# Kernel tuning notes

Hardware: AMD Instinct MI355X
Metric: run time of the kernel (lower is better)

The kernel has to match this reference:

```python
import jax, jax.numpy as jnp
import numpy as np

OUT_F = 4096
IN_F = 4096
NUM_BITS = 4
BLOCK = 64
R = 16
LORA_SCALE = 32.0 / R  # lora_alpha / r


def setup_inputs() -> dict:
    key = jax.random.key(0)
    k1, k2, k3, k4, k5, k6 = jax.random.split(key, 6)
    n_packed = OUT_F * IN_F * NUM_BITS // 8  # bytes; 2 nibbles per byte
    n_blocks = OUT_F * IN_F // BLOCK
    return {
        "x": jax.random.normal(k1, (2, 1024, IN_F), dtype=jnp.float32),
        "qweight": jax.random.randint(k2, (n_packed,), 0, 256, dtype=jnp.int32),
        "scales": jax.random.uniform(k3, (n_blocks,), dtype=jnp.float32),
        "bias": jax.random.normal(k4, (OUT_F,), dtype=jnp.float32),
        "lora_A": jax.random.normal(k5, (R, IN_F), dtype=jnp.float32) * 0.02,
        "lora_B": jax.random.normal(k6, (OUT_F, R), dtype=jnp.float32) * 0.02,
    }


def _dequantize(qweight, scales):
    # uniform 4-bit lookup table: linspace(-1, 1, 16)
    table = jnp.linspace(-1.0, 1.0, 2 ** NUM_BITS).astype(scales.dtype)
    mask = (1 << NUM_BITS) - 1
    # unpack: index i stored at bits [i*NUM_BITS, (i+1)*NUM_BITS) of each byte
    lo = qweight & mask
    hi = (qweight >> NUM_BITS) & mask
    idx = jnp.stack([lo, hi], axis=-1).reshape(-1)  # [OUT_F*IN_F]
    vals = table[idx]                                # gather from lookup table
    # per-block rescale, then reshape to [OUT_F, IN_F]
    w = vals.reshape(-1, BLOCK) * scales[:, None]
    return w.reshape(OUT_F, IN_F)


def reference(x, qweight, scales, bias, lora_A, lora_B):
    W = _dequantize(qweight, scales)                      # [out, in]
    base = jnp.einsum('bsi,oi->bso', x, W) + bias          # F.linear
    lora = jnp.einsum('bsr,or->bso', jnp.einsum('bsi,ri->bsr', x, lora_A), lora_B)
    return base + LORA_SCALE * lora
```

## Files before the change

kernel.cpp:

```cpp
#include <hip/hip_runtime.h>
#include <hip/hip_bf16.h>
#include <stdint.h>

#define IN_F   4096
#define OUT_F  4096
#define M_ROWS 2048
#define LORA_SCALE 2.0f

typedef __bf16 bf16x8 __attribute__((ext_vector_type(8)));
typedef float  f32x4  __attribute__((ext_vector_type(4)));

typedef const __attribute__((address_space(1))) void gvoid_t;
typedef __attribute__((address_space(3))) void lvoid_t;

#define WAITVM(n) __builtin_amdgcn_s_waitcnt(((n)&0xF) | (((n)>>4)<<14) | (7<<4) | (15<<8))

__global__ void dequant_kernel(const int* __restrict__ qw,
                               const float* __restrict__ scales,
                               __hip_bfloat16* __restrict__ W) {
    int t = blockIdx.x * 256 + threadIdx.x;
    int4 q = ((const int4*)qw)[t];
    float scale = scales[t >> 3];
    float step = scale * (2.0f / 15.0f);
    int bb[4] = {q.x, q.y, q.z, q.w};
    union { __hip_bfloat16 h[8]; uint4 v; } o;
    #pragma unroll
    for (int j = 0; j < 4; ++j) {
        float lo = (float)(bb[j] & 15)        * step - scale;
        float hi = (float)((bb[j] >> 4) & 15) * step - scale;
        o.h[2*j]   = __float2bfloat16(lo);
        o.h[2*j+1] = __float2bfloat16(hi);
    }
    ((uint4*)W)[t] = o.v;
}

__global__ void xcast_kernel(const float* __restrict__ x,
                             __hip_bfloat16* __restrict__ xb) {
    int t = blockIdx.x * 256 + threadIdx.x;
    float4 a = ((const float4*)x)[2*t];
    float4 c = ((const float4*)x)[2*t + 1];
    union { __hip_bfloat16 h[8]; uint4 v; } o;
    o.h[0] = __float2bfloat16(a.x); o.h[1] = __float2bfloat16(a.y);
    o.h[2] = __float2bfloat16(a.z); o.h[3] = __float2bfloat16(a.w);
    o.h[4] = __float2bfloat16(c.x); o.h[5] = __float2bfloat16(c.y);
    o.h[6] = __float2bfloat16(c.z); o.h[7] = __float2bfloat16(c.w);
    ((uint4*)xb)[t] = o.v;
}

__global__ void lora_kernel(const float* __restrict__ x,
                            const float* __restrict__ A,
                            float* __restrict__ tout) {
    __shared__ float red[16 * 4 * 16];
    int m0 = blockIdx.x * 4;
    int r = threadIdx.x & 15;
    int g = threadIdx.x >> 4;
    float acc[4] = {0.f, 0.f, 0.f, 0.f};
    const float* ar = A + (size_t)r * IN_F;
    for (int kb = 0; kb < 32; ++kb) {
        int k = kb * 128 + g * 8;
        float4 a0 = *(const float4*)(ar + k);
        float4 a1 = *(const float4*)(ar + k + 4);
        #pragma unroll
        for (int row = 0; row < 4; ++row) {
            float4 x0 = *(const float4*)(x + (size_t)(m0 + row) * IN_F + k);
            float4 x1 = *(const float4*)(x + (size_t)(m0 + row) * IN_F + k + 4);
            acc[row] += x0.x*a0.x + x0.y*a0.y + x0.z*a0.z + x0.w*a0.w
                      + x1.x*a1.x + x1.y*a1.y + x1.z*a1.z + x1.w*a1.w;
        }
    }
    #pragma unroll
    for (int row = 0; row < 4; ++row) red[g*64 + row*16 + r] = acc[row];
    __syncthreads();
    if (threadIdx.x < 64) {
        int row = threadIdx.x >> 4, rr = threadIdx.x & 15;
        float s = 0.f;
        #pragma unroll
        for (int gg = 0; gg < 16; ++gg) s += red[gg*64 + row*16 + rr];
        tout[(size_t)(m0 + row) * 16 + rr] = s;
    }
}

__global__ __launch_bounds__(256) void gemm_kernel(
        const __hip_bfloat16* __restrict__ A,
        const __hip_bfloat16* __restrict__ B,
        const float* __restrict__ bias,
        const float* __restrict__ loraB,
        const float* __restrict__ tmat,
        float* __restrict__ out) {
    const int K = IN_F, N = OUT_F;
    __shared__ union alignas(16) {
        struct { __hip_bfloat16 As[4][128*32]; __hip_bfloat16 Bs[4][128*32]; } s;
        float tl[128 * 16];
    } sm;

    int tid  = threadIdx.x;
    int wave = tid >> 6, lane = tid & 63;
    int wm = wave >> 1, wn = wave & 1;
    int row16 = lane & 15, quad = lane >> 4;

    int lin = blockIdx.y * 32 + blockIdx.x;
    int xcd = lin & 7, slot = lin >> 3;
    int bx = (xcd & 3) * 8 + (slot & 7);
    int by = (xcd >> 2) * 8 + (slot >> 3);
    int m0 = by * 128, n0 = bx * 128;

    int rl = lane >> 2;
    int cg = (lane & 3) ^ ((rl >> 1) & 3);

    const __hip_bfloat16* pA0 = A + (size_t)(m0 + wave*32 + rl) * K + cg*8;
    const __hip_bfloat16* pA1 = pA0 + (size_t)16 * K;
    const __hip_bfloat16* pB0 = B + (size_t)(n0 + wave*32 + rl) * K + cg*8;
    const __hip_bfloat16* pB1 = pB0 + (size_t)16 * K;

    f32x4 acc[4][4];
    #pragma unroll
    for (int i = 0; i < 4; ++i)
        #pragma unroll
        for (int j = 0; j < 4; ++j) acc[i][j] = (f32x4){0.f, 0.f, 0.f, 0.f};

    #define DMA(buf)                                                              \
        __builtin_amdgcn_global_load_lds((gvoid_t*)pA0, (lvoid_t*)&sm.s.As[buf][(wave*2+0)*512], 16, 0, 0); \
        __builtin_amdgcn_global_load_lds((gvoid_t*)pA1, (lvoid_t*)&sm.s.As[buf][(wave*2+1)*512], 16, 0, 0); \
        __builtin_amdgcn_global_load_lds((gvoid_t*)pB0, (lvoid_t*)&sm.s.Bs[buf][(wave*2+0)*512], 16, 0, 0); \
        __builtin_amdgcn_global_load_lds((gvoid_t*)pB1, (lvoid_t*)&sm.s.Bs[buf][(wave*2+1)*512], 16, 0, 0); \
        pA0 += 32; pA1 += 32; pB0 += 32; pB1 += 32;

    #define COMPUTE(buf)                                                          \
    {                                                                             \
        bf16x8 af[4], bfr[4];                                                     \
        _Pragma("unroll")                                                         \
        for (int mt = 0; mt < 4; ++mt) {                                          \
            int row = wm*64 + mt*16 + row16;                                      \
            af[mt] = *(const bf16x8*)&sm.s.As[buf][row*32 + ((quad ^ ((row>>1)&3)) << 3)]; \
        }                                                                         \
        _Pragma("unroll")                                                         \
        for (int nt = 0; nt < 4; ++nt) {                                          \
            int row = wn*64 + nt*16 + row16;                                      \
            bfr[nt] = *(const bf16x8*)&sm.s.Bs[buf][row*32 + ((quad ^ ((row>>1)&3)) << 3)]; \
        }                                                                         \
        _Pragma("unroll")                                                         \
        for (int mt = 0; mt < 4; ++mt)                                            \
            _Pragma("unroll")                                                     \
            for (int nt = 0; nt < 4; ++nt)                                        \
                acc[mt][nt] = __builtin_amdgcn_mfma_f32_16x16x32_bf16(            \
                    af[mt], bfr[nt], acc[mt][nt], 0, 0, 0);                       \
    }

    #define STEP(p)                                                               \
        WAITVM(8);                                  \
        __builtin_amdgcn_s_barrier();       \
        __builtin_amdgcn_sched_barrier(0);                                        \
        COMPUTE(p)                                                                \
        DMA((p+3)&3)

    DMA(0)
    DMA(1)
    DMA(2)

    for (int u = 0; u < 31; ++u) {
        STEP(0)
        STEP(1)
        STEP(2)
        STEP(3)
    }
    STEP(0)
    WAITVM(8); __builtin_amdgcn_s_barrier(); __builtin_amdgcn_sched_barrier(0);
    COMPUTE(1)
    WAITVM(4); __builtin_amdgcn_s_barrier(); __builtin_amdgcn_sched_barrier(0);
    COMPUTE(2)
    WAITVM(0); __builtin_amdgcn_s_barrier(); __builtin_amdgcn_sched_barrier(0);
    COMPUTE(3)

    #undef STEP
    #undef COMPUTE
    #undef DMA

    #pragma unroll
    for (int i = 0; i < 2; ++i)
        ((float4*)sm.tl)[tid + i*256] =
            ((const float4*)(tmat + (size_t)m0 * 16))[tid + i*256];
    __syncthreads();

    #pragma unroll
    for (int nt = 0; nt < 4; ++nt) {
        int n = n0 + wn*64 + nt*16 + row16;
        float bn = bias[n];
        const float4* lb = (const float4*)(loraB + (size_t)n * 16);
        float4 b0 = lb[0], b1 = lb[1], b2 = lb[2], b3 = lb[3];
        #pragma unroll
        for (int mt = 0; mt < 4; ++mt) {
            #pragma unroll
            for (int r = 0; r < 4; ++r) {
                int ml = wm*64 + mt*16 + quad*4 + r;
                const float* tm = &sm.tl[ml * 16];
                float dot =
                    tm[0]*b0.x + tm[1]*b0.y + tm[2]*b0.z + tm[3]*b0.w +
                    tm[4]*b1.x + tm[5]*b1.y + tm[6]*b1.z + tm[7]*b1.w +
                    tm[8]*b2.x + tm[9]*b2.y + tm[10]*b2.z + tm[11]*b2.w +
                    tm[12]*b3.x + tm[13]*b3.y + tm[14]*b3.z + tm[15]*b3.w;
                out[(size_t)(m0 + ml) * N + n] = acc[mt][nt][r] + bn + LORA_SCALE * dot;
            }
        }
    }
}

extern "C" void kernel_launch(void* const* d_in, const int* in_sizes, int n_in,
                              void* d_out, int out_size, void* d_ws, size_t ws_size,
                              hipStream_t stream) {
    const float* x      = (const float*)d_in[0];
    const int*   qw     = (const int*)d_in[1];
    const float* scales = (const float*)d_in[2];
    const float* bias   = (const float*)d_in[3];
    const float* loraA  = (const float*)d_in[4];
    const float* loraB  = (const float*)d_in[5];
    float* out = (float*)d_out;

    char* ws = (char*)d_ws;
    __hip_bfloat16* Wb = (__hip_bfloat16*)ws;
    __hip_bfloat16* Xb = (__hip_bfloat16*)(ws + 33554432);
    float* tmat        = (float*)(ws + 50331648);

    dequant_kernel<<<8192, 256, 0, stream>>>(qw, scales, Wb);
    xcast_kernel<<<4096, 256, 0, stream>>>(x, Xb);
    lora_kernel<<<512, 256, 0, stream>>>(x, loraA, tmat);
    gemm_kernel<<<dim3(32, 16), 256, 0, stream>>>(Xb, Wb, bias, loraB, tmat, out);
}
```

Measured before the change: 272.7 us.

## Fuse 4-bit dequantization into GEMM B-tile loads via packed nibble repack

Replaces the full bf16 dequant pass with a repack kernel that compresses the int32-per-byte weights into packed nibbles. The GEMM then streams the 4-bit words into LDS and dequantizes them in registers using per-block scales, which are preloaded and transposed into shared memory. The aim is to avoid writing and re-reading a 32 MB bf16 weight matrix and to cut the GEMM's B-side bandwidth. In exchange it adds ALU conversion work inside the MFMA loop, uses more LDS for the scales, and makes each B load a 4-byte DMA.

```diff
diff --git a/kernel.cpp b/kernel.cpp
--- a/kernel.cpp
+++ b/kernel.cpp
@@ -15,23 +15,21 @@
 
 #define WAITVM(n) __builtin_amdgcn_s_waitcnt(((n)&0xF) | (((n)>>4)<<14) | (7<<4) | (15<<8))
 
-__global__ void dequant_kernel(const int* __restrict__ qw,
-                               const float* __restrict__ scales,
-                               __hip_bfloat16* __restrict__ W) {
+__global__ void repack_kernel(const int* __restrict__ qw,
+                              uint32_t* __restrict__ qp) {
     int t = blockIdx.x * 256 + threadIdx.x;
-    int4 q = ((const int4*)qw)[t];
-    float scale = scales[t >> 3];
-    float step = scale * (2.0f / 15.0f);
-    int bb[4] = {q.x, q.y, q.z, q.w};
-    union { __hip_bfloat16 h[8]; uint4 v; } o;
-    #pragma unroll
-    for (int j = 0; j < 4; ++j) {
-        float lo = (float)(bb[j] & 15)        * step - scale;
-        float hi = (float)((bb[j] >> 4) & 15) * step - scale;
-        o.h[2*j]   = __float2bfloat16(lo);
-        o.h[2*j+1] = __float2bfloat16(hi);
-    }
-    ((uint4*)W)[t] = o.v;
+    const int4* src = (const int4*)qw + 4 * (size_t)t;
+    int4 a = src[0], b = src[1], c = src[2], d = src[3];
+    uint4 o;
+    o.x = (uint32_t)(a.x & 255) | ((uint32_t)(a.y & 255) << 8) |
+          ((uint32_t)(a.z & 255) << 16) | ((uint32_t)(a.w & 255) << 24);
+    o.y = (uint32_t)(b.x & 255) | ((uint32_t)(b.y & 255) << 8) |
+          ((uint32_t)(b.z & 255) << 16) | ((uint32_t)(b.w & 255) << 24);
+    o.z = (uint32_t)(c.x & 255) | ((uint32_t)(c.y & 255) << 8) |
+          ((uint32_t)(c.z & 255) << 16) | ((uint32_t)(c.w & 255) << 24);
+    o.w = (uint32_t)(d.x & 255) | ((uint32_t)(d.y & 255) << 8) |
+          ((uint32_t)(d.z & 255) << 16) | ((uint32_t)(d.w & 255) << 24);
+    ((uint4*)qp)[t] = o;
 }
 
 __global__ void xcast_kernel(const float* __restrict__ x,
@@ -82,14 +80,19 @@
 
 __global__ __launch_bounds__(256) void gemm_kernel(
         const __hip_bfloat16* __restrict__ A,
-        const __hip_bfloat16* __restrict__ B,
+        const uint32_t* __restrict__ Bq,
+        const float* __restrict__ scales,
         const float* __restrict__ bias,
         const float* __restrict__ loraB,
         const float* __restrict__ tmat,
         float* __restrict__ out) {
     const int K = IN_F, N = OUT_F;
     __shared__ union alignas(16) {
-        struct { __hip_bfloat16 As[4][128*32]; __hip_bfloat16 Bs[4][128*32]; } s;
+        struct {
+            __hip_bfloat16 As[4][128*32];
+            uint32_t       Bp[4][128*4];
+            float          scl[64*128];
+        } s;
         float tl[128 * 16];
     } sm;
 
@@ -109,21 +112,46 @@
 
     const __hip_bfloat16* pA0 = A + (size_t)(m0 + wave*32 + rl) * K + cg*8;
     const __hip_bfloat16* pA1 = pA0 + (size_t)16 * K;
-    const __hip_bfloat16* pB0 = B + (size_t)(n0 + wave*32 + rl) * K + cg*8;
-    const __hip_bfloat16* pB1 = pB0 + (size_t)16 * K;
+    const uint32_t* pB0 = Bq + (size_t)(n0 + wave*32 + rl) * 512 + (lane & 3);
+    const uint32_t* pB1 = pB0 + (size_t)16 * 512;
+
+    {
+        const float* sg = scales + (size_t)n0 * 64;
+        int r2 = tid >> 1;
+        int c2 = (tid & 1) * 32;
+        const float* src = sg + (size_t)r2 * 64 + c2;
+        #pragma unroll
+        for (int j = 0; j < 32; j += 4) {
+            float4 v = *(const float4*)(src + j);
+            sm.s.scl[(c2 + j + 0)*128 + r2] = v.x;
+            sm.s.scl[(c2 + j + 1)*128 + r2] = v.y;
+            sm.s.scl[(c2 + j + 2)*128 + r2] = v.z;
+            sm.s.scl[(c2 + j + 3)*128 + r2] = v.w;
+        }
+    }
+    __syncthreads();
 
     f32x4 acc[4][4];
     #pragma unroll
     for (int i = 0; i < 4; ++i)
         #pragma unroll
         for (int j = 0; j < 4; ++j) acc[i][j] = (f32x4){0.f, 0.f, 0.f, 0.f};
+
+    float scl_r[4], step_r[4];
+
+    #define SCALES(kb)                                                            \
+        _Pragma("unroll")                                                         \
+        for (int nt = 0; nt < 4; ++nt) {                                          \
+            float sv = sm.s.scl[(kb)*128 + wn*64 + nt*16 + row16];                \
+            scl_r[nt] = sv; step_r[nt] = sv * (2.0f / 15.0f);                     \
+        }
 
     #define DMA(buf)                                                              \
         __builtin_amdgcn_global_load_lds((gvoid_t*)pA0, (lvoid_t*)&sm.s.As[buf][(wave*2+0)*512], 16, 0, 0); \
         __builtin_amdgcn_global_load_lds((gvoid_t*)pA1, (lvoid_t*)&sm.s.As[buf][(wave*2+1)*512], 16, 0, 0); \
-        __builtin_amdgcn_global_load_lds((gvoid_t*)pB0, (lvoid_t*)&sm.s.Bs[buf][(wave*2+0)*512], 16, 0, 0); \
-        __builtin_amdgcn_global_load_lds((gvoid_t*)pB1, (lvoid_t*)&sm.s.Bs[buf][(wave*2+1)*512], 16, 0, 0); \
-        pA0 += 32; pA1 += 32; pB0 += 32; pB1 += 32;
+        __builtin_amdgcn_global_load_lds((gvoid_t*)pB0, (lvoid_t*)&sm.s.Bp[buf][wave*128],      4, 0, 0);  \
+        __builtin_amdgcn_global_load_lds((gvoid_t*)pB1, (lvoid_t*)&sm.s.Bp[buf][wave*128 + 64], 4, 0, 0);  \
+        pA0 += 32; pA1 += 32; pB0 += 4; pB1 += 4;
 
     #define COMPUTE(buf)                                                          \
     {                                                                             \
@@ -136,7 +164,14 @@
         _Pragma("unroll")                                                         \
         for (int nt = 0; nt < 4; ++nt) {                                          \
             int row = wn*64 + nt*16 + row16;                                      \
-            bfr[nt] = *(const bf16x8*)&sm.s.Bs[buf][row*32 + ((quad ^ ((row>>1)&3)) << 3)]; \
+            uint32_t pw = sm.s.Bp[buf][row*4 + quad];                             \
+            float st = step_r[nt], sc = scl_r[nt];                                \
+            union { __hip_bfloat16 h[8]; bf16x8 v; } u;                           \
+            _Pragma("unroll")                                                     \
+            for (int j = 0; j < 8; ++j)                                           \
+                u.h[j] = __float2bfloat16(                                        \
+                    fmaf((float)((pw >> (4*j)) & 15u), st, -sc));                 \
+            bfr[nt] = u.v;                                                        \
         }                                                                         \
         _Pragma("unroll")                                                         \
         for (int mt = 0; mt < 4; ++mt)                                            \
@@ -158,14 +193,18 @@
     DMA(2)
 
     for (int u = 0; u < 31; ++u) {
+        SCALES(2*u)
         STEP(0)
         STEP(1)
+        SCALES(2*u + 1)
         STEP(2)
         STEP(3)
     }
+    SCALES(62)
     STEP(0)
     WAITVM(8); __builtin_amdgcn_s_barrier(); __builtin_amdgcn_sched_barrier(0);
     COMPUTE(1)
+    SCALES(63)
     WAITVM(4); __builtin_amdgcn_s_barrier(); __builtin_amdgcn_sched_barrier(0);
     COMPUTE(2)
     WAITVM(0); __builtin_amdgcn_s_barrier(); __builtin_amdgcn_sched_barrier(0);
@@ -174,6 +213,7 @@
     #undef STEP
     #undef COMPUTE
     #undef DMA
+    #undef SCALES
 
     #pragma unroll
     for (int i = 0; i < 2; ++i)
@@ -216,12 +256,12 @@
     float* out = (float*)d_out;
 
     char* ws = (char*)d_ws;
-    __hip_bfloat16* Wb = (__hip_bfloat16*)ws;
+    uint32_t* qp       = (uint32_t*)ws;
     __hip_bfloat16* Xb = (__hip_bfloat16*)(ws + 33554432);
     float* tmat        = (float*)(ws + 50331648);
 
-    dequant_kernel<<<8192, 256, 0, stream>>>(qw, scales, Wb);
+    repack_kernel<<<2048, 256, 0, stream>>>(qw, qp);
     xcast_kernel<<<4096, 256, 0, stream>>>(x, Xb);
     lora_kernel<<<512, 256, 0, stream>>>(x, loraA, tmat);
-    gemm_kernel<<<dim3(32, 16), 256, 0, stream>>>(Xb, Wb, bias, loraB, tmat, out);
-}
+    gemm_kernel<<<dim3(32, 16), 256, 0, stream>>>(Xb, qp, scales, bias, loraB, tmat, out);
+}
```

Result: slower. 323.8 us (+18.7%).
